# Performance work log

Hardware: AMD Instinct MI355X
Metric: run time of the kernel (lower is better)

Reference implementation:

```python
import jax, jax.numpy as jnp
import numpy as np

B, H, S, P = 4, 16, 1024, 64
D = H * P  # state_size = 1024


def setup_inputs() -> dict:
    key = jax.random.key(0)
    k0, k1, k2, k3, k4 = jax.random.split(key, 5)
    q = jax.random.normal(k0, (B * H, S, P), jnp.float32)
    k = jax.random.normal(k1, (B * H, S, P), jnp.float32)
    v = jax.random.normal(k2, (B * H, S, P), jnp.float32)
    # xavier_uniform for the merge projection (fan_in = fan_out = D)
    limit = np.sqrt(6.0 / (D + D)).astype(np.float32)
    w_merge = jax.random.uniform(k3, (D, D), jnp.float32, -limit, limit)
    # causal position mask: True = masked (as used by masked_fill)
    position_mask = jnp.triu(jnp.ones((S, S), dtype=bool), k=1)
    # source-length padding mask: True = padded position
    lengths = jax.random.randint(k4, (B,), S // 2, S + 1)
    src_length_mask = jnp.arange(S)[None, :] >= lengths[:, None]
    return {"q": q, "k": k, "v": v, "w_merge": w_merge,
            "position_mask": position_mask, "src_length_mask": src_length_mask}


def reference(q, k, v, w_merge, position_mask, src_length_mask):
    # q,k,v: [B*H, S, P]; position_mask: [S,S] bool; src_length_mask: [B,S] bool
    BH, T, Pp = q.shape
    nb = src_length_mask.shape[0]
    nh = BH // nb
    scale = 1.0 / np.sqrt(Pp).astype(np.float32)
    # logits = bmm(q, k^T) * scale
    logits = jnp.einsum('btp,bsp->bts', q, k) * scale  # [B*H, T, S]
    logits = logits.reshape(nb, nh, T, T)
    logits = jnp.where(position_mask[None, None, :, :], -jnp.inf, logits)
    logits = jnp.where(src_length_mask[:, None, None, :], -jnp.inf, logits)
    scores = jax.nn.softmax(logits, axis=-1).reshape(BH, T, T)
    # dropout is identity in eval / p=0
    data = jnp.einsum('bts,bsp->btp', scores, v)  # [B*H, T, P]
    # merge heads: [B, H, T, P] -> [B, T, H*P]
    data = data.reshape(nb, nh, T, Pp).transpose(0, 2, 1, 3).reshape(nb, T, nh * Pp)
    return data @ w_merge.T  # Linear(bias=False)
```

## Files before the change

kernel.cpp:

```cpp
#include <hip/hip_runtime.h>
#include <hip/hip_bf16.h>
#include <math.h>


typedef _Float16 f16x8 __attribute__((ext_vector_type(8)));
typedef unsigned short u16x8 __attribute__((ext_vector_type(8)));
typedef float f32x4 __attribute__((ext_vector_type(4)));

union H8 { u16x8 u; f16x8 h; };

static __device__ __forceinline__ unsigned short f2hu(float f) {
  _Float16 h = (_Float16)f;
  unsigned short u;
  __builtin_memcpy(&u, &h, 2);
  return u;
}

#define MFMA16(a, b, c) __builtin_amdgcn_mfma_f32_16x16x32_f16((a), (b), (c), 0, 0, 0)

static __device__ __forceinline__ void gload16(const void* g, void* l) {
  __builtin_amdgcn_global_load_lds(
      (const __attribute__((address_space(1))) unsigned int*)g,
      (__attribute__((address_space(3))) unsigned int*)l, 16, 0, 0);
}

__global__ __launch_bounds__(256) void prep_all(const float* __restrict__ w,
                                                const int* __restrict__ smask,
                                                const float* __restrict__ kin,
                                                const float* __restrict__ vin,
                                                unsigned short* __restrict__ w_h,
                                                unsigned short* __restrict__ k_sw,
                                                unsigned short* __restrict__ v_sw,
                                                int* __restrict__ lengths) {
  const int bid = blockIdx.x;
  const int tid = threadIdx.x;
  if (bid < 4) {
    __shared__ int sh[256];
    int4 m = ((const int4*)(smask + bid * 1024))[tid];
    sh[tid] = (m.x != 0) + (m.y != 0) + (m.z != 0) + (m.w != 0);
    __syncthreads();
    for (int o = 128; o > 0; o >>= 1) {
      if (tid < o) sh[tid] += sh[tid + o];
      __syncthreads();
    }
    if (tid == 0) lengths[bid] = 1024 - sh[0];
  } else if (bid < 1028) {
    int idx = (bid - 4) * 256 + tid;
    float4 f = ((const float4*)w)[idx];
    ushort4 o;
    o.x = f2hu(f.x); o.y = f2hu(f.y); o.z = f2hu(f.z); o.w = f2hu(f.w);
    ((ushort4*)w_h)[idx] = o;
  } else if (bid < 3076) {
    int idx = (bid - 1028) * 256 + tid;
    const float4* src = ((const float4*)kin) + (size_t)idx * 2;
    float4 a = src[0], b = src[1];
    u16x8 o;
    o[0] = f2hu(a.x); o[1] = f2hu(a.y); o[2] = f2hu(a.z); o[3] = f2hu(a.w);
    o[4] = f2hu(b.x); o[5] = f2hu(b.y); o[6] = f2hu(b.z); o[7] = f2hu(b.w);
    int bh = idx >> 13;
    int i = idx & 8191;
    int s = i >> 3;
    int c16 = i & 7;
    int kt = s >> 6, r = s & 63;
    int xb = (r * 128 + c16 * 16) ^ ((r & 7) << 4);
    *(u16x8*)((char*)k_sw + ((size_t)(bh * 16 + kt)) * 8192 + xb) = o;
  } else {
    const int t = bid - 3076;
    const int bh = t >> 4;
    const int st = t & 15;
    __shared__ unsigned short T[64][72];
    const float* vp = vin + ((size_t)bh * 1024 + st * 64) * 64;
#pragma unroll
    for (int i = 0; i < 4; ++i) {
      int e = i * 256 + tid;
      int row = e >> 4;
      int c4 = (e & 15) * 4;
      float4 f = *(const float4*)(vp + row * 64 + c4);
      T[c4 + 0][row] = f2hu(f.x);
      T[c4 + 1][row] = f2hu(f.y);
      T[c4 + 2][row] = f2hu(f.z);
      T[c4 + 3][row] = f2hu(f.w);
    }
    __syncthreads();
#pragma unroll
    for (int i = 0; i < 4; ++i) {
      int e = i * 256 + tid;
      int feat = e >> 4;
      int c4 = (e & 15) * 4;
      ushort4 o;
      o.x = T[feat][c4 + 0]; o.y = T[feat][c4 + 1];
      o.z = T[feat][c4 + 2]; o.w = T[feat][c4 + 3];
      int xb = (feat * 128 + c4 * 2) ^ ((feat & 7) << 4);
      *(ushort4*)((char*)v_sw + ((size_t)(bh * 16 + st)) * 8192 + xb) = o;
    }
  }
}

static __device__ __forceinline__ void qset_step(const unsigned short* Kcur,
                                                 const unsigned short* Vcur,
                                                 char* Pw, const H8 qa[2],
                                                 f32x4 (&oacc)[4], f32x4& sumacc,
                                                 int kt, int qbase, int len,
                                                 int l15, int kgrp, int wv) {
  f32x4 sacc[4] = {};
  __builtin_amdgcn_s_setprio(1);
#pragma unroll
  for (int kb = 0; kb < 2; kb++)
#pragma unroll
    for (int nb = 0; nb < 4; nb++) {
      H8 bb;
      bb.u = *(const u16x8*)((const char*)Kcur +
              (((nb * 16 + l15) * 128 + (kb * 32 + kgrp * 8) * 2) ^ ((l15 & 7) << 4)));
      sacc[nb] = MFMA16(qa[kb].h, bb.h, sacc[nb]);
    }
  __builtin_amdgcn_s_setprio(0);

#pragma unroll
  for (int nb = 0; nb < 4; nb++) {
    int scol = kt * 64 + nb * 16 + l15;
#pragma unroll
    for (int r = 0; r < 4; r++) {
      int trow = qbase + wv * 16 + kgrp * 4 + r;
      float pv = (scol > trow || scol >= len)
                     ? 0.f
                     : __expf(fmaf(sacc[nb][r], 0.125f, -5.0f));
      int prow = kgrp * 4 + r;
      int pcol = nb * 16 + l15;
      *(unsigned short*)(Pw + ((prow * 128 + pcol * 2) ^ ((prow & 7) << 4))) = f2hu(pv);
    }
  }

  const f16x8 ones_h = {(_Float16)1.f, (_Float16)1.f, (_Float16)1.f, (_Float16)1.f,
                        (_Float16)1.f, (_Float16)1.f, (_Float16)1.f, (_Float16)1.f};
  __builtin_amdgcn_s_setprio(1);
#pragma unroll
  for (int kb = 0; kb < 2; kb++) {
    H8 pa;
    pa.u = *(const u16x8*)((const char*)Pw +
            ((l15 * 128 + (kb * 32 + kgrp * 8) * 2) ^ ((l15 & 7) << 4)));
    sumacc = MFMA16(pa.h, ones_h, sumacc);
#pragma unroll
    for (int nb = 0; nb < 4; nb++) {
      H8 vb;
      vb.u = *(const u16x8*)((const char*)Vcur +
              (((nb * 16 + l15) * 128 + (kb * 32 + kgrp * 8) * 2) ^ ((l15 & 7) << 4)));
      oacc[nb] = MFMA16(pa.h, vb.h, oacc[nb]);
    }
  }
  __builtin_amdgcn_s_setprio(0);
}

__global__ __launch_bounds__(256, 2) void attn_pair(const float* __restrict__ q,
                                                    const unsigned short* __restrict__ k_sw,
                                                    const unsigned short* __restrict__ v_sw,
                                                    const int* __restrict__ lengths,
                                                    unsigned short* __restrict__ attn_out) {
  const int wg = blockIdx.x;
  const int idx = (wg & 7) * 64 + (wg >> 3);
  const int bh = idx >> 3;
  const int p = idx & 7;
  const int qtA = p;
  const int qtB = 15 - p;
  const int b = bh >> 4;
  const int h = bh & 15;
  const int tid = threadIdx.x;
  const int lane = tid & 63;
  const int wv = tid >> 6;
  const int l15 = lane & 15;
  const int kgrp = lane >> 4;
  const int qbaseA = qtA * 64;
  const int qbaseB = qtB * 64;
  const int len = lengths[b];

  __shared__ __align__(16) unsigned short Kb[3][4096];
  __shared__ __align__(16) unsigned short Vb[3][4096];
  __shared__ __align__(16) unsigned short Plds[4][2][1024];

  const char* kbase_sw = (const char*)k_sw + (size_t)bh * 16 * 8192;
  const char* vbase_sw = (const char*)v_sw + (size_t)bh * 16 * 8192;
  char* PwA = (char*)(&Plds[wv][0][0]);
  char* PwB = (char*)(&Plds[wv][1][0]);

  H8 qaA[2], qaB[2];
  {
    const float* qpA = q + ((size_t)bh * 1024 + qbaseA + wv * 16 + l15) * 64;
    const float* qpB = q + ((size_t)bh * 1024 + qbaseB + wv * 16 + l15) * 64;
#pragma unroll
    for (int kb = 0; kb < 2; kb++) {
      const float* a0 = qpA + kb * 32 + kgrp * 8;
      float4 f0 = *(const float4*)(a0);
      float4 f1 = *(const float4*)(a0 + 4);
      u16x8 u;
      u[0] = f2hu(f0.x); u[1] = f2hu(f0.y); u[2] = f2hu(f0.z); u[3] = f2hu(f0.w);
      u[4] = f2hu(f1.x); u[5] = f2hu(f1.y); u[6] = f2hu(f1.z); u[7] = f2hu(f1.w);
      qaA[kb].u = u;
      const float* b0 = qpB + kb * 32 + kgrp * 8;
      float4 g0 = *(const float4*)(b0);
      float4 g1 = *(const float4*)(b0 + 4);
      u16x8 vv;
      vv[0] = f2hu(g0.x); vv[1] = f2hu(g0.y); vv[2] = f2hu(g0.z); vv[3] = f2hu(g0.w);
      vv[4] = f2hu(g1.x); vv[5] = f2hu(g1.y); vv[6] = f2hu(g1.z); vv[7] = f2hu(g1.w);
      qaB[kb].u = vv;
    }
  }

  f32x4 oaccA[4] = {}, oaccB[4] = {};
  f32x4 sumA = {}, sumB = {};

  const int nktA = qtA + 1;
  const int capB = (len - 1 < qbaseB + 63) ? (len - 1) : (qbaseB + 63);
  const int nktB = (capB >> 6) + 1;

#define STAGE_T(t, buf)                                                      \
  do {                                                                       \
    const char* ks_ = kbase_sw + (size_t)(t) * 8192;                         \
    const char* vs_ = vbase_sw + (size_t)(t) * 8192;                         \
    _Pragma("unroll") for (int j = 0; j < 2; ++j) {                          \
      int ch = wv * 2 + j;                                                   \
      gload16(ks_ + ch * 1024 + lane * 16, (char*)Kb[buf] + ch * 1024);      \
      gload16(vs_ + ch * 1024 + lane * 16, (char*)Vb[buf] + ch * 1024);      \
    }                                                                        \
  } while (0)

  STAGE_T(0, 0);
  STAGE_T(1, 1);

  for (int kt = 0; kt < nktB; ++kt) {
    const int cur = kt % 3;
    if (kt + 1 < nktB) {
      asm volatile("s_waitcnt vmcnt(4)" ::: "memory");
    } else {
      asm volatile("s_waitcnt vmcnt(0)" ::: "memory");
    }
    __builtin_amdgcn_s_barrier();
    if (kt + 2 < nktB) {
      const int nbuf = (kt + 2) % 3;
      STAGE_T(kt + 2, nbuf);
    }

    qset_step(Kb[cur], Vb[cur], PwB, qaB, oaccB, sumB, kt, qbaseB, len, l15, kgrp, wv);
    if (kt < nktA)
      qset_step(Kb[cur], Vb[cur], PwA, qaA, oaccA, sumA, kt, qbaseA, len, l15, kgrp, wv);
  }
#undef STAGE_T

#pragma unroll
  for (int nb = 0; nb < 4; nb++)
#pragma unroll
    for (int r = 0; r < 4; r++) {
      int feat = nb * 16 + l15;
      int trowA = qbaseA + wv * 16 + kgrp * 4 + r;
      attn_out[((size_t)b * 1024 + trowA) * 1024 + h * 64 + feat] =
          f2hu(oaccA[nb][r] / sumA[r]);
      int trowB = qbaseB + wv * 16 + kgrp * 4 + r;
      attn_out[((size_t)b * 1024 + trowB) * 1024 + h * 64 + feat] =
          f2hu(oaccB[nb][r] / sumB[r]);
    }
}

__global__ __launch_bounds__(256) void merge_kernel(const unsigned short* __restrict__ a_h,
                                                    const unsigned short* __restrict__ w_h,
                                                    float* __restrict__ out) {
  const int n0 = blockIdx.x * 64;
  const int m0 = blockIdx.y * 64;
  const int tid = threadIdx.x;
  const int lane = tid & 63;
  const int wv = tid >> 6;
  const int l15 = lane & 15;
  const int kgrp = lane >> 4;

  __shared__ unsigned short Alds[64 * 64];
  __shared__ unsigned short Wlds[64 * 64];

  f32x4 acc[4] = {};

  for (int kt = 0; kt < 16; ++kt) {
    __syncthreads();
#pragma unroll
    for (int i = 0; i < 4; i++) {
      int e = i * 256 + tid;
      int row = e >> 4;
      int c4 = (e & 15) * 4;
      ushort4 av = *(const ushort4*)(a_h + (size_t)(m0 + row) * 1024 + kt * 64 + c4);
      *(ushort4*)((char*)Alds + ((row * 128 + c4 * 2) ^ ((row & 7) << 4))) = av;
      ushort4 wv4 = *(const ushort4*)(w_h + (size_t)(n0 + row) * 1024 + kt * 64 + c4);
      *(ushort4*)((char*)Wlds + ((row * 128 + c4 * 2) ^ ((row & 7) << 4))) = wv4;
    }
    __syncthreads();
#pragma unroll
    for (int kb = 0; kb < 2; kb++) {
      int arow = wv * 16 + l15;
      H8 aa;
      aa.u = *(const u16x8*)((const char*)Alds +
                             ((arow * 128 + (kb * 32 + kgrp * 8) * 2) ^ ((arow & 7) << 4)));
#pragma unroll
      for (int nb = 0; nb < 4; nb++) {
        int wrow = nb * 16 + l15;
        H8 bb;
        bb.u = *(const u16x8*)((const char*)Wlds +
                               ((wrow * 128 + (kb * 32 + kgrp * 8) * 2) ^ ((wrow & 7) << 4)));
        acc[nb] = MFMA16(aa.h, bb.h, acc[nb]);
      }
    }
  }
#pragma unroll
  for (int nb = 0; nb < 4; nb++)
#pragma unroll
    for (int r = 0; r < 4; r++)
      out[(size_t)(m0 + wv * 16 + kgrp * 4 + r) * 1024 + n0 + nb * 16 + l15] = acc[nb][r];
}

extern "C" void kernel_launch(void* const* d_in, const int* in_sizes, int n_in,
                              void* d_out, int out_size, void* d_ws, size_t ws_size,
                              hipStream_t stream) {
  const float* q = (const float*)d_in[0];
  const float* k = (const float*)d_in[1];
  const float* v = (const float*)d_in[2];
  const float* w = (const float*)d_in[3];
  const int* smask = (const int*)d_in[5];
  float* out = (float*)d_out;

  char* ws = (char*)d_ws;
  const size_t MB = 1024 * 1024;
  int* lengths = (int*)ws;
  unsigned short* w_h = (unsigned short*)(ws + 256);
  unsigned short* attn_h = (unsigned short*)(ws + 256 + 2 * MB);
  unsigned short* k_sw = (unsigned short*)(ws + 256 + 10 * MB);
  unsigned short* v_sw = (unsigned short*)(ws + 256 + 18 * MB);

  hipLaunchKernelGGL(prep_all, dim3(4100), dim3(256), 0, stream,
                     w, smask, k, v, w_h, k_sw, v_sw, lengths);
  hipLaunchKernelGGL(attn_pair, dim3(512), dim3(256), 0, stream,
                     q, k_sw, v_sw, lengths, attn_h);
  hipLaunchKernelGGL(merge_kernel, dim3(16, 64), dim3(256), 0, stream, attn_h, w_h, out);
}
```

Baseline: 65.05 us.

## Pre-swizzle merge operands into tiles and pipeline merge GEMM with async LDS loads

```diff
diff --git a/kernel.cpp b/kernel.cpp
--- a/kernel.cpp
+++ b/kernel.cpp
@@ -28,7 +28,7 @@
                                                 const int* __restrict__ smask,
                                                 const float* __restrict__ kin,
                                                 const float* __restrict__ vin,
-                                                unsigned short* __restrict__ w_h,
+                                                unsigned short* __restrict__ w_sw,
                                                 unsigned short* __restrict__ k_sw,
                                                 unsigned short* __restrict__ v_sw,
                                                 int* __restrict__ lengths) {
@@ -49,7 +49,11 @@
     float4 f = ((const float4*)w)[idx];
     ushort4 o;
     o.x = f2hu(f.x); o.y = f2hu(f.y); o.z = f2hu(f.z); o.w = f2hu(f.w);
-    ((ushort4*)w_h)[idx] = o;
+    int row = idx >> 8;
+    int c4 = (idx & 255) * 4;
+    int nt = row >> 6, r = row & 63, kt = c4 >> 6, cb = (c4 & 63) * 2;
+    *(ushort4*)((char*)w_sw + ((size_t)(nt * 16 + kt)) * 8192 +
+                ((r * 128 + cb) ^ ((r & 7) << 4))) = o;
   } else if (bid < 3076) {
     int idx = (bid - 1028) * 256 + tid;
     const float4* src = ((const float4*)kin) + (size_t)idx * 2;
@@ -150,11 +154,21 @@
   __builtin_amdgcn_s_setprio(0);
 }
 
+static __device__ __forceinline__ void store_attn_sw(unsigned short* attn_sw,
+                                                     int b, int h, int trow,
+                                                     int nb, int l15, float v) {
+  int grow = b * 1024 + trow;
+  int mt = grow >> 7, rr = grow & 127;
+  int cb = (nb * 16 + l15) * 2;
+  *(unsigned short*)((char*)attn_sw + ((size_t)(mt * 16 + h)) * 16384 +
+                     ((rr * 128 + cb) ^ ((rr & 7) << 4))) = f2hu(v);
+}
+
 __global__ __launch_bounds__(256, 2) void attn_pair(const float* __restrict__ q,
                                                     const unsigned short* __restrict__ k_sw,
                                                     const unsigned short* __restrict__ v_sw,
                                                     const int* __restrict__ lengths,
-                                                    unsigned short* __restrict__ attn_out) {
+                                                    unsigned short* __restrict__ attn_sw) {
   const int wg = blockIdx.x;
   const int idx = (wg & 7) * 64 + (wg >> 3);
   const int bh = idx >> 3;
@@ -248,66 +262,95 @@
   for (int nb = 0; nb < 4; nb++)
 #pragma unroll
     for (int r = 0; r < 4; r++) {
-      int feat = nb * 16 + l15;
       int trowA = qbaseA + wv * 16 + kgrp * 4 + r;
-      attn_out[((size_t)b * 1024 + trowA) * 1024 + h * 64 + feat] =
-          f2hu(oaccA[nb][r] / sumA[r]);
+      store_attn_sw(attn_sw, b, h, trowA, nb, l15, oaccA[nb][r] / sumA[r]);
       int trowB = qbaseB + wv * 16 + kgrp * 4 + r;
-      attn_out[((size_t)b * 1024 + trowB) * 1024 + h * 64 + feat] =
-          f2hu(oaccB[nb][r] / sumB[r]);
-    }
-}
-
-__global__ __launch_bounds__(256) void merge_kernel(const unsigned short* __restrict__ a_h,
-                                                    const unsigned short* __restrict__ w_h,
-                                                    float* __restrict__ out) {
-  const int n0 = blockIdx.x * 64;
-  const int m0 = blockIdx.y * 64;
+      store_attn_sw(attn_sw, b, h, trowB, nb, l15, oaccB[nb][r] / sumB[r]);
+    }
+}
+
+__global__ __launch_bounds__(256, 2) void merge_sw(const unsigned short* __restrict__ a_sw,
+                                                   const unsigned short* __restrict__ w_sw,
+                                                   float* __restrict__ out) {
+  const int mt = blockIdx.x;
+  const int nt = blockIdx.y;
   const int tid = threadIdx.x;
   const int lane = tid & 63;
   const int wv = tid >> 6;
   const int l15 = lane & 15;
   const int kgrp = lane >> 4;
-
-  __shared__ unsigned short Alds[64 * 64];
-  __shared__ unsigned short Wlds[64 * 64];
-
-  f32x4 acc[4] = {};
-
-  for (int kt = 0; kt < 16; ++kt) {
-    __syncthreads();
-#pragma unroll
-    for (int i = 0; i < 4; i++) {
-      int e = i * 256 + tid;
-      int row = e >> 4;
-      int c4 = (e & 15) * 4;
-      ushort4 av = *(const ushort4*)(a_h + (size_t)(m0 + row) * 1024 + kt * 64 + c4);
-      *(ushort4*)((char*)Alds + ((row * 128 + c4 * 2) ^ ((row & 7) << 4))) = av;
-      ushort4 wv4 = *(const ushort4*)(w_h + (size_t)(n0 + row) * 1024 + kt * 64 + c4);
-      *(ushort4*)((char*)Wlds + ((row * 128 + c4 * 2) ^ ((row & 7) << 4))) = wv4;
-    }
-    __syncthreads();
+  const int wr = wv >> 1;
+  const int wc = wv & 1;
+
+  __shared__ __align__(16) unsigned short Ab[3][8192];
+  __shared__ __align__(16) unsigned short Wb[3][4096];
+
+  const char* abase = (const char*)a_sw + (size_t)mt * 16 * 16384;
+  const char* wbase = (const char*)w_sw + (size_t)nt * 16 * 8192;
+
+  f32x4 acc[4][2] = {};
+
+#define MSTAGE(t, buf)                                                    \
+  do {                                                                    \
+    const char* as_ = abase + (size_t)(t) * 16384;                        \
+    const char* ws_ = wbase + (size_t)(t) * 8192;                         \
+    _Pragma("unroll") for (int j = 0; j < 4; ++j) {                       \
+      int ch = wv * 4 + j;                                                \
+      gload16(as_ + ch * 1024 + lane * 16, (char*)Ab[buf] + ch * 1024);   \
+    }                                                                     \
+    _Pragma("unroll") for (int j = 0; j < 2; ++j) {                       \
+      int ch = wv * 2 + j;                                                \
+      gload16(ws_ + ch * 1024 + lane * 16, (char*)Wb[buf] + ch * 1024);   \
+    }                                                                     \
+  } while (0)
+
+  MSTAGE(0, 0);
+  MSTAGE(1, 1);
+
+  for (int t = 0; t < 16; ++t) {
+    const int cur = t % 3;
+    if (t + 1 < 16) {
+      asm volatile("s_waitcnt vmcnt(6)" ::: "memory");
+    } else {
+      asm volatile("s_waitcnt vmcnt(0)" ::: "memory");
+    }
+    __builtin_amdgcn_s_barrier();
+    if (t + 2 < 16) MSTAGE(t + 2, (t + 2) % 3);
+
+    __builtin_amdgcn_s_setprio(1);
 #pragma unroll
     for (int kb = 0; kb < 2; kb++) {
-      int arow = wv * 16 + l15;
-      H8 aa;
-      aa.u = *(const u16x8*)((const char*)Alds +
-                             ((arow * 128 + (kb * 32 + kgrp * 8) * 2) ^ ((arow & 7) << 4)));
-#pragma unroll
-      for (int nb = 0; nb < 4; nb++) {
-        int wrow = nb * 16 + l15;
-        H8 bb;
-        bb.u = *(const u16x8*)((const char*)Wlds +
-                               ((wrow * 128 + (kb * 32 + kgrp * 8) * 2) ^ ((wrow & 7) << 4)));
-        acc[nb] = MFMA16(aa.h, bb.h, acc[nb]);
+      H8 wf[2];
+#pragma unroll
+      for (int nb = 0; nb < 2; nb++) {
+        int wrow = wc * 32 + nb * 16 + l15;
+        wf[nb].u = *(const u16x8*)((const char*)Wb[cur] +
+                    ((wrow * 128 + (kb * 32 + kgrp * 8) * 2) ^ ((wrow & 7) << 4)));
       }
-    }
-  }
-#pragma unroll
-  for (int nb = 0; nb < 4; nb++)
-#pragma unroll
-    for (int r = 0; r < 4; r++)
-      out[(size_t)(m0 + wv * 16 + kgrp * 4 + r) * 1024 + n0 + nb * 16 + l15] = acc[nb][r];
+#pragma unroll
+      for (int mb = 0; mb < 4; mb++) {
+        int arow = wr * 64 + mb * 16 + l15;
+        H8 aa;
+        aa.u = *(const u16x8*)((const char*)Ab[cur] +
+                ((arow * 128 + (kb * 32 + kgrp * 8) * 2) ^ ((arow & 7) << 4)));
+#pragma unroll
+        for (int nb = 0; nb < 2; nb++)
+          acc[mb][nb] = MFMA16(aa.h, wf[nb].h, acc[mb][nb]);
+      }
+    }
+    __builtin_amdgcn_s_setprio(0);
+  }
+#undef MSTAGE
+
+  const int m0 = mt * 128, n0 = nt * 64;
+#pragma unroll
+  for (int mb = 0; mb < 4; mb++)
+#pragma unroll
+    for (int nb = 0; nb < 2; nb++)
+#pragma unroll
+      for (int r = 0; r < 4; r++)
+        out[(size_t)(m0 + wr * 64 + mb * 16 + kgrp * 4 + r) * 1024 +
+            n0 + wc * 32 + nb * 16 + l15] = acc[mb][nb][r];
 }
 
 extern "C" void kernel_launch(void* const* d_in, const int* in_sizes, int n_in,
@@ -323,14 +366,14 @@
   char* ws = (char*)d_ws;
   const size_t MB = 1024 * 1024;
   int* lengths = (int*)ws;
-  unsigned short* w_h = (unsigned short*)(ws + 256);
-  unsigned short* attn_h = (unsigned short*)(ws + 256 + 2 * MB);
+  unsigned short* w_sw = (unsigned short*)(ws + 256);
+  unsigned short* attn_sw = (unsigned short*)(ws + 256 + 2 * MB);
   unsigned short* k_sw = (unsigned short*)(ws + 256 + 10 * MB);
   unsigned short* v_sw = (unsigned short*)(ws + 256 + 18 * MB);
 
   hipLaunchKernelGGL(prep_all, dim3(4100), dim3(256), 0, stream,
-                     w, smask, k, v, w_h, k_sw, v_sw, lengths);
+                     w, smask, k, v, w_sw, k_sw, v_sw, lengths);
   hipLaunchKernelGGL(attn_pair, dim3(512), dim3(256), 0, stream,
-                     q, k_sw, v_sw, lengths, attn_h);
-  hipLaunchKernelGGL(merge_kernel, dim3(16, 64), dim3(256), 0, stream, attn_h, w_h, out);
-}
+                     q, k_sw, v_sw, lengths, attn_sw);
+  hipLaunchKernelGGL(merge_sw, dim3(32, 16), dim3(256), 0, stream, attn_sw, w_sw, out);
+}
```

Result: faster. 58.16 us (-10.6%).
